# Performance work log

Hardware: AMD Instinct MI355X
Metric: run time of the kernel (lower is better)

Reference implementation:

```python
import jax, jax.numpy as jnp
import numpy as np

H = 2048      # hidden_size
I = 768       # moe_intermediate_size
E = 32        # num_experts
K = 8         # num_experts_per_tok (top_k)
T = 1024      # tokens (batch * seq)


def setup_inputs() -> dict:
    key = jax.random.key(0)
    k1, k2, k3, k4 = jax.random.split(key, 4)
    return {
        "hidden_states": jax.random.normal(k1, (T, H), jnp.float32),
        "gate_weight": jax.random.normal(k2, (E, H), jnp.float32) * 0.02,
        "w13_weight": jax.random.normal(k3, (E, 2 * I, H), jnp.float32) * 0.02,
        "w2_weight": jax.random.normal(k4, (E, H, I), jnp.float32) * 0.02,
    }


def reference(hidden_states, gate_weight, w13_weight, w2_weight):
    x = hidden_states  # [T, H]
    # --- router (Qwen3MoeSparseMoeBlock gating) ---
    logits = x @ gate_weight.T                      # [T, E]
    probs = jax.nn.softmax(logits, axis=-1)
    topk_w, topk_idx = jax.lax.top_k(probs, K)      # [T, K]
    topk_w = topk_w / jnp.sum(topk_w, axis=-1, keepdims=True)  # norm_topk_prob
    # dense combine matrix [T, E]: routing weight per (token, expert), 0 if not selected
    combine = jnp.zeros((x.shape[0], E), x.dtype).at[
        jnp.arange(x.shape[0])[:, None], topk_idx
    ].add(topk_w)
    # --- expert FFNs (fused gate+up = w13, SiLU-gated, then w2 down-proj) ---
    h = jnp.einsum('th,eoh->eto', x, w13_weight)    # [E, T, 2I]
    gate, up = h[:, :, :I], h[:, :, I:]
    act = jax.nn.silu(gate) * up                    # [E, T, I]
    y = jnp.einsum('eti,ehi->eth', act, w2_weight)  # [E, T, H]
    # --- weighted combine ---
    return jnp.einsum('eth,te->th', y, combine)     # [T, H]
```

## Files before the change

### kernel.cpp

```cpp
#include <hip/hip_runtime.h>
#include <hip/hip_bf16.h>
#include <math.h>

#define T_TOK 1024
#define H_DIM 2048
#define I_DIM 768
#define E_NUM 32
#define K_TOP 8
#define BK 32
#define GRID_P 1024

typedef __bf16 bf16x8 __attribute__((ext_vector_type(8)));
typedef float  f32x4  __attribute__((ext_vector_type(4)));

__device__ __forceinline__ bf16x8 cvt2_bf16(const f32x4 a, const f32x4 b) {
    bf16x8 r;
    r[0] = (__bf16)a[0]; r[1] = (__bf16)a[1]; r[2] = (__bf16)a[2]; r[3] = (__bf16)a[3];
    r[4] = (__bf16)b[0]; r[5] = (__bf16)b[1]; r[6] = (__bf16)b[2]; r[7] = (__bf16)b[3];
    return r;
}

__device__ __forceinline__ int frag_off(int r, int kgrp8) {
    return (r >> 4) * 512 + kgrp8 * 128 + (r & 15) * 8;
}

__global__ __launch_bounds__(256) void zero_kernel(float* __restrict__ p)
{
    const int i = (blockIdx.x * 256 + threadIdx.x) * 4;
    *(f32x4*)(p + i) = f32x4{0.f, 0.f, 0.f, 0.f};
}

__global__ __launch_bounds__(256) void cvtx_kernel(
    const float* __restrict__ x, __bf16* __restrict__ xb)
{
    const int i = (blockIdx.x * 256 + threadIdx.x) * 8;
    const f32x4 a = *(const f32x4*)(x + i);
    const f32x4 b = *(const f32x4*)(x + i + 4);
    *(bf16x8*)(xb + i) = cvt2_bf16(a, b);
}

__global__ __launch_bounds__(256) void router_kernel(
    const float* __restrict__ x, const float* __restrict__ gw,
    float* __restrict__ wdense, unsigned int* __restrict__ masks)
{
    const int t = blockIdx.x;
    const int tid = threadIdx.x;
    __shared__ float part[256];
    __shared__ float logits[E_NUM];
    const int e = tid & 31;
    const int chunk = tid >> 5;
    const float* xr = x + (size_t)t * H_DIM;
    const float* gr = gw + (size_t)e * H_DIM;
    const int base = chunk * (H_DIM / 8);
    float s = 0.f;
    for (int h = 0; h < H_DIM / 8; h += 4) {
        const f32x4 xv = *reinterpret_cast<const f32x4*>(xr + base + h);
        const f32x4 gv = *reinterpret_cast<const f32x4*>(gr + base + h);
        s += xv[0]*gv[0] + xv[1]*gv[1] + xv[2]*gv[2] + xv[3]*gv[3];
    }
    part[tid] = s;
    __syncthreads();
    if (tid < E_NUM) {
        float tot = 0.f;
        for (int c = 0; c < 8; ++c) tot += part[c * 32 + tid];
        logits[tid] = tot;
    }
    __syncthreads();
    if (tid == 0) {
        float l[E_NUM];
        for (int i = 0; i < E_NUM; ++i) {
            l[i] = logits[i];
            wdense[(size_t)t * E_NUM + i] = 0.f;
        }
        unsigned mask = 0;
        int   idx[K_TOP];
        float lv[K_TOP];
        for (int k = 0; k < K_TOP; ++k) {
            float best = -1e30f; int bi = 0;
            for (int i = 0; i < E_NUM; ++i)
                if (!((mask >> i) & 1u) && l[i] > best) { best = l[i]; bi = i; }
            mask |= (1u << bi); idx[k] = bi; lv[k] = best;
        }
        const float m = lv[0];
        float den = 0.f;
        for (int k = 0; k < K_TOP; ++k) den += expf(lv[k] - m);
        for (int k = 0; k < K_TOP; ++k)
            wdense[(size_t)t * E_NUM + idx[k]] = expf(lv[k] - m) / den;
        masks[t] = mask;
    }
}

__global__ __launch_bounds__(256) void count_kernel(
    const unsigned int* __restrict__ masks, int* __restrict__ cnt)
{
    const int e = blockIdx.x;
    const int tid = threadIdx.x;
    int c = 0;
    for (int t = tid; t < T_TOK; t += 256) c += (masks[t] >> e) & 1u;
    __shared__ int red[256];
    red[tid] = c; __syncthreads();
    for (int s = 128; s > 0; s >>= 1) {
        if (tid < s) red[tid] += red[tid + s];
        __syncthreads();
    }
    if (tid == 0) cnt[e] = red[0];
}

__global__ void scan_kernel(const int* __restrict__ cnt, int* __restrict__ off,
                            int* __restrict__ tbl)
{
    if (threadIdx.x == 0 && blockIdx.x == 0) {
        int r = 0, nt = 0;
        for (int e = 0; e < E_NUM; ++e) {
            off[e] = r;
            const int c = cnt[e];
            r += c;
            const int t = (c + 127) >> 7;
            for (int z = 0; z < t; ++z) tbl[1 + nt++] = (e << 8) | z;
        }
        tbl[0] = nt;
    }
}

__global__ __launch_bounds__(256) void fill_kernel(
    const unsigned int* __restrict__ masks, const float* __restrict__ wdense,
    const int* __restrict__ off, int* __restrict__ tok, float* __restrict__ wgt)
{
    const int e = blockIdx.x;
    const int tid = threadIdx.x;
    const int PER = T_TOK / 256;
    int sel[PER]; int c = 0;
    for (int i = 0; i < PER; ++i) {
        const int t = tid * PER + i;
        sel[i] = (masks[t] >> e) & 1u;
        c += sel[i];
    }
    __shared__ int s[256];
    s[tid] = c; __syncthreads();
    if (tid == 0) {
        int r = 0;
        for (int j = 0; j < 256; ++j) { int v = s[j]; s[j] = r; r += v; }
    }
    __syncthreads();
    int pos = off[e] + s[tid];
    for (int i = 0; i < PER; ++i) {
        if (sel[i]) {
            const int t = tid * PER + i;
            tok[pos] = t;
            wgt[pos] = wdense[(size_t)t * E_NUM + e];
            pos++;
        }
    }
}

#define G1_PHASE(P, Q)                                                         \
  {                                                                            \
    if (scur + 2 < NS) {                                                       \
      const int kk = (scur + 2) * BK;                                          \
      pa##P##_0 = *(const bf16x8*)(xp + kk);                                   \
      pa##P##_1 = *(const bf16x8*)(xp + kk + 8);                               \
      pb##P##_0 = *(const f32x4*)(wp + kk);                                    \
      pb##P##_1 = *(const f32x4*)(wp + kk + 4);                                \
      pb##P##_2 = *(const f32x4*)(wp + kk + 8);                                \
      pb##P##_3 = *(const f32x4*)(wp + kk + 12);                               \
    }                                                                          \
    bf16x8 af[4], bfr[4];                                                      \
    _Pragma("unroll")                                                          \
    for (int m = 0; m < 4; ++m)                                                \
      af[m] = *(const bf16x8*)&As[P][((wm >> 4) + m) * 512 + lane * 8];        \
    _Pragma("unroll")                                                          \
    for (int n = 0; n < 4; ++n)                                                \
      bfr[n] = *(const bf16x8*)&Bs[P][(wn * 4 + n) * 512 + lane * 8];          \
    _Pragma("unroll")                                                          \
    for (int m = 0; m < 4; ++m)                                                \
      _Pragma("unroll")                                                        \
      for (int n = 0; n < 4; ++n)                                              \
        acc[m][n] = __builtin_amdgcn_mfma_f32_16x16x32_bf16(af[m], bfr[n],     \
                                                            acc[m][n], 0,0,0); \
    if (scur + 1 < NS) {                                                       \
      *(bf16x8*)&As[Q][wo]       = pa##Q##_0;                                  \
      *(bf16x8*)&As[Q][wo + 128] = pa##Q##_1;                                  \
      *(bf16x8*)&Bs[Q][wo]       = cvt2_bf16(pb##Q##_0, pb##Q##_1);            \
      *(bf16x8*)&Bs[Q][wo + 128] = cvt2_bf16(pb##Q##_2, pb##Q##_3);            \
    }                                                                          \
    asm volatile("s_waitcnt lgkmcnt(0)" ::: "memory");                         \
    __builtin_amdgcn_s_barrier();                                              \
    ++scur;                                                                    \
  }

__global__ __launch_bounds__(256, 3) void gemm1_kernel(
    const __bf16* __restrict__ xb, const float* __restrict__ w13,
    const int* __restrict__ tok, const int* __restrict__ cnt,
    const int* __restrict__ off, const int* __restrict__ tbl,
    unsigned short* __restrict__ act)
{
    __shared__ __bf16 As[2][4096];
    __shared__ __bf16 Bs[2][4096];
    const int tid  = threadIdx.x;
    const int wid  = tid >> 6;
    const int lane = tid & 63;
    const int wm = (wid >> 1) * 64;
    const int wn = (wid & 1);
    const int lrow = lane & 15;
    const int sr = tid >> 1;
    const int kh = tid & 1;
    const int wo = frag_off(sr, kh * 2);
    const int NS = H_DIM / BK;

    const int W = tbl[0] * 12;
    for (int w = blockIdx.x; w < W; w += gridDim.x) {
        const int ti   = w / 12;
        const int nidx = w - ti * 12;
        const int ez = tbl[1 + ti];
        const int e  = ez >> 8;
        const int m0 = (ez & 255) * 128;
        const int c  = cnt[e];
        const int o  = off[e];
        const int n0 = nidx * 64;

        int rA = m0 + sr; rA = rA < c ? rA : c - 1;
        const __bf16* xp = xb + (size_t)tok[o + rA] * H_DIM + kh * 16;
        const int grp = sr >> 5;
        const int wrow = (grp & 1) * I_DIM + n0 + (grp >> 1) * 32 + (sr & 31);
        const float* wp = w13 + (size_t)e * (2 * I_DIM) * H_DIM
                              + (size_t)wrow * H_DIM + kh * 16;

        bf16x8 pa0_0, pa0_1, pa1_0, pa1_1;
        f32x4  pb0_0, pb0_1, pb0_2, pb0_3, pb1_0, pb1_1, pb1_2, pb1_3;
        f32x4  acc[4][4] = {};

        pa0_0 = *(const bf16x8*)(xp);
        pa0_1 = *(const bf16x8*)(xp + 8);
        pb0_0 = *(const f32x4*)(wp);
        pb0_1 = *(const f32x4*)(wp + 4);
        pb0_2 = *(const f32x4*)(wp + 8);
        pb0_3 = *(const f32x4*)(wp + 12);
        pa1_0 = *(const bf16x8*)(xp + BK);
        pa1_1 = *(const bf16x8*)(xp + BK + 8);
        pb1_0 = *(const f32x4*)(wp + BK);
        pb1_1 = *(const f32x4*)(wp + BK + 4);
        pb1_2 = *(const f32x4*)(wp + BK + 8);
        pb1_3 = *(const f32x4*)(wp + BK + 12);
        *(bf16x8*)&As[0][wo]       = pa0_0;
        *(bf16x8*)&As[0][wo + 128] = pa0_1;
        *(bf16x8*)&Bs[0][wo]       = cvt2_bf16(pb0_0, pb0_1);
        *(bf16x8*)&Bs[0][wo + 128] = cvt2_bf16(pb0_2, pb0_3);
        asm volatile("s_waitcnt lgkmcnt(0)" ::: "memory");
        __builtin_amdgcn_s_barrier();

        int scur = 0;
        for (int it = 0; it < NS; it += 2) {
            G1_PHASE(0, 1)
            G1_PHASE(1, 0)
        }

#pragma unroll
        for (int m = 0; m < 4; ++m)
#pragma unroll
            for (int n = 0; n < 2; ++n)
#pragma unroll
                for (int i = 0; i < 4; ++i) {
                    const int row = m0 + wm + m * 16 + (lane >> 4) * 4 + i;
                    if (row < c) {
                        const int icol = n0 + wn * 32 + n * 16 + lrow;
                        const float g = acc[m][n][i];
                        const float u = acc[m][n + 2][i];
                        const float a = (g / (1.f + expf(-g))) * u;
                        act[(size_t)(o + row) * I_DIM + icol] =
                            __builtin_bit_cast(unsigned short, (__bf16)a);
                    }
                }
    }
}

#define G2_PHASE(P, Q)                                                         \
  {                                                                            \
    if (scur + 2 < NS) {                                                       \
      const int kk = (scur + 2) * BK;                                          \
      qa##P##_0 = *(const bf16x8*)(ap + kk);                                   \
      qa##P##_1 = *(const bf16x8*)(ap + kk + 8);                               \
      qb##P##_0 = *(const f32x4*)(wp + kk);                                    \
      qb##P##_1 = *(const f32x4*)(wp + kk + 4);                                \
      qb##P##_2 = *(const f32x4*)(wp + kk + 8);                                \
      qb##P##_3 = *(const f32x4*)(wp + kk + 12);                               \
    }                                                                          \
    bf16x8 af[4], bfr[4];                                                      \
    _Pragma("unroll")                                                          \
    for (int m = 0; m < 4; ++m)                                                \
      af[m] = *(const bf16x8*)&As[P][((wm >> 4) + m) * 512 + lane * 8];        \
    _Pragma("unroll")                                                          \
    for (int n = 0; n < 4; ++n)                                                \
      bfr[n] = *(const bf16x8*)&Bs[P][(wn * 4 + n) * 512 + lane * 8];          \
    _Pragma("unroll")                                                          \
    for (int m = 0; m < 4; ++m)                                                \
      _Pragma("unroll")                                                        \
      for (int n = 0; n < 4; ++n)                                              \
        acc[m][n] = __builtin_amdgcn_mfma_f32_16x16x32_bf16(af[m], bfr[n],     \
                                                            acc[m][n], 0,0,0); \
    if (scur + 1 < NS) {                                                       \
      *(bf16x8*)&As[Q][wo]       = qa##Q##_0;                                  \
      *(bf16x8*)&As[Q][wo + 128] = qa##Q##_1;                                  \
      *(bf16x8*)&Bs[Q][wo]       = cvt2_bf16(qb##Q##_0, qb##Q##_1);            \
      *(bf16x8*)&Bs[Q][wo + 128] = cvt2_bf16(qb##Q##_2, qb##Q##_3);            \
    }                                                                          \
    asm volatile("s_waitcnt lgkmcnt(0)" ::: "memory");                         \
    __builtin_amdgcn_s_barrier();                                              \
    ++scur;                                                                    \
  }

__global__ __launch_bounds__(256, 3) void gemm2_kernel(
    const unsigned short* __restrict__ act, const float* __restrict__ w2,
    const int* __restrict__ tok, const float* __restrict__ wgt,
    const int* __restrict__ cnt, const int* __restrict__ off,
    const int* __restrict__ tbl, float* __restrict__ out)
{
    __shared__ __bf16 As[2][4096];
    __shared__ __bf16 Bs[2][4096];
    const int tid  = threadIdx.x;
    const int wid  = tid >> 6;
    const int lane = tid & 63;
    const int wm = (wid >> 1) * 64;
    const int wn = (wid & 1);
    const int lrow = lane & 15;
    const int sr = tid >> 1;
    const int kh = tid & 1;
    const int wo = frag_off(sr, kh * 2);
    const int NS = I_DIM / BK;

    const int W = tbl[0] * 16;
    for (int w = blockIdx.x; w < W; w += gridDim.x) {
        const int ti   = w >> 4;
        const int nidx = w & 15;
        const int ez = tbl[1 + ti];
        const int e  = ez >> 8;
        const int m0 = (ez & 255) * 128;
        const int c  = cnt[e];
        const int o  = off[e];
        const int n0 = nidx * 128;

        int rA = m0 + sr; rA = rA < c ? rA : c - 1;
        const __bf16* ap = (const __bf16*)act + (size_t)(o + rA) * I_DIM + kh * 16;
        const float* wp = w2 + (size_t)e * H_DIM * I_DIM
                             + (size_t)(n0 + sr) * I_DIM + kh * 16;

        bf16x8 qa0_0, qa0_1, qa1_0, qa1_1;
        f32x4  qb0_0, qb0_1, qb0_2, qb0_3, qb1_0, qb1_1, qb1_2, qb1_3;
        f32x4  acc[4][4] = {};

        qa0_0 = *(const bf16x8*)(ap);
        qa0_1 = *(const bf16x8*)(ap + 8);
        qb0_0 = *(const f32x4*)(wp);
        qb0_1 = *(const f32x4*)(wp + 4);
        qb0_2 = *(const f32x4*)(wp + 8);
        qb0_3 = *(const f32x4*)(wp + 12);
        qa1_0 = *(const bf16x8*)(ap + BK);
        qa1_1 = *(const bf16x8*)(ap + BK + 8);
        qb1_0 = *(const f32x4*)(wp + BK);
        qb1_1 = *(const f32x4*)(wp + BK + 4);
        qb1_2 = *(const f32x4*)(wp + BK + 8);
        qb1_3 = *(const f32x4*)(wp + BK + 12);
        *(bf16x8*)&As[0][wo]       = qa0_0;
        *(bf16x8*)&As[0][wo + 128] = qa0_1;
        *(bf16x8*)&Bs[0][wo]       = cvt2_bf16(qb0_0, qb0_1);
        *(bf16x8*)&Bs[0][wo + 128] = cvt2_bf16(qb0_2, qb0_3);
        asm volatile("s_waitcnt lgkmcnt(0)" ::: "memory");
        __builtin_amdgcn_s_barrier();

        int scur = 0;
        for (int it = 0; it < NS; it += 2) {
            G2_PHASE(0, 1)
            G2_PHASE(1, 0)
        }

#pragma unroll
        for (int m = 0; m < 4; ++m)
#pragma unroll
            for (int n = 0; n < 4; ++n)
#pragma unroll
                for (int i = 0; i < 4; ++i) {
                    const int row = m0 + wm + m * 16 + (lane >> 4) * 4 + i;
                    if (row < c) {
                        const int t = tok[o + row];
                        const float wv = wgt[o + row];
                        const int hcol = n0 + wn * 64 + n * 16 + lrow;
                        atomicAdd(&out[(size_t)t * H_DIM + hcol], wv * acc[m][n][i]);
                    }
                }
    }
}

extern "C" void kernel_launch(void* const* d_in, const int* in_sizes, int n_in,
                              void* d_out, int out_size, void* d_ws, size_t ws_size,
                              hipStream_t stream)
{
    const float* x   = (const float*)d_in[0];
    const float* gw  = (const float*)d_in[1];
    const float* w13 = (const float*)d_in[2];
    const float* w2  = (const float*)d_in[3];
    float* out = (float*)d_out;

    char* ws = (char*)d_ws;
    float*          wdense = (float*)(ws + 0x00000);
    unsigned int*   masks  = (unsigned int*)(ws + 0x20000);
    int*            cnt    = (int*)(ws + 0x21000);
    int*            off    = (int*)(ws + 0x21800);
    int*            tbl    = (int*)(ws + 0x22000);
    int*            tok    = (int*)(ws + 0x23000);
    float*          wgt    = (float*)(ws + 0x2B000);
    unsigned short* act    = (unsigned short*)(ws + 0x33000);
    __bf16*         xb     = (__bf16*)(ws + 0xC40000);

    zero_kernel<<<(T_TOK * H_DIM) / (256 * 4), 256, 0, stream>>>(out);

    cvtx_kernel<<<(T_TOK * H_DIM) / (256 * 8), 256, 0, stream>>>(x, xb);
    router_kernel<<<T_TOK, 256, 0, stream>>>(x, gw, wdense, masks);
    count_kernel<<<E_NUM, 256, 0, stream>>>(masks, cnt);
    scan_kernel<<<1, 64, 0, stream>>>(cnt, off, tbl);
    fill_kernel<<<E_NUM, 256, 0, stream>>>(masks, wdense, off, tok, wgt);
    gemm1_kernel<<<GRID_P, 256, 0, stream>>>(xb, w13, tok, cnt, off, tbl, act);
    gemm2_kernel<<<GRID_P, 256, 0, stream>>>(act, w2, tok, wgt, cnt, off, tbl, out);
}
```

Before: 384.5 us.

## Load A fragments directly from global into registers, swizzle B LDS layout

Both expert GEMMs now skip staging the activation (A) operand in shared memory. Each lane loads its MFMA A fragments straight from global memory into registers, double-buffered across k-steps. The B tile in LDS gets an XOR swizzle to reduce bank conflicts, gemm2's occupancy hint rises to 4, and gemm1's grid drops to 768 blocks. The aim is less LDS traffic and footprint, at the cost of redundant, less-coalesced global A loads across waves that share rows.

```diff
diff --git a/kernel.cpp b/kernel.cpp
--- a/kernel.cpp
+++ b/kernel.cpp
@@ -8,10 +8,11 @@
 #define E_NUM 32
 #define K_TOP 8
 #define BK 32
-#define GRID_P 1024
 
 typedef __bf16 bf16x8 __attribute__((ext_vector_type(8)));
 typedef float  f32x4  __attribute__((ext_vector_type(4)));
+
+#define MFMA16(a, b, c) __builtin_amdgcn_mfma_f32_16x16x32_bf16((a), (b), (c), 0, 0, 0)
 
 __device__ __forceinline__ bf16x8 cvt2_bf16(const f32x4 a, const f32x4 b) {
     bf16x8 r;
@@ -22,6 +23,9 @@
 
 __device__ __forceinline__ int frag_off(int r, int kgrp8) {
     return (r >> 4) * 512 + kgrp8 * 128 + (r & 15) * 8;
+}
+__device__ __forceinline__ int swz(int e) {
+    return e ^ (((e >> 8) & 3) << 3);
 }
 
 __global__ __launch_bounds__(256) void zero_kernel(float* __restrict__ p)
@@ -153,48 +157,67 @@
     }
 }
 
-#define G1_PHASE(P, Q)                                                         \
+#define GEMM_PHASE(P, Q)                                                       \
   {                                                                            \
+    bf16x8 bfr[4];                                                             \
+    _Pragma("unroll")                                                          \
+    for (int n = 0; n < 4; ++n)                                                \
+      bfr[n] = *(const bf16x8*)&Bs[P][swz((wn * 4 + n) * 512 + lane * 8)];     \
+    _Pragma("unroll")                                                          \
+    for (int n = 0; n < 4; ++n) {                                              \
+      acc[0][n] = MFMA16(a##P##0, bfr[n], acc[0][n]);                          \
+      acc[1][n] = MFMA16(a##P##1, bfr[n], acc[1][n]);                          \
+      acc[2][n] = MFMA16(a##P##2, bfr[n], acc[2][n]);                          \
+      acc[3][n] = MFMA16(a##P##3, bfr[n], acc[3][n]);                          \
+    }                                                                          \
     if (scur + 2 < NS) {                                                       \
       const int kk = (scur + 2) * BK;                                          \
-      pa##P##_0 = *(const bf16x8*)(xp + kk);                                   \
-      pa##P##_1 = *(const bf16x8*)(xp + kk + 8);                               \
-      pb##P##_0 = *(const f32x4*)(wp + kk);                                    \
-      pb##P##_1 = *(const f32x4*)(wp + kk + 4);                                \
-      pb##P##_2 = *(const f32x4*)(wp + kk + 8);                                \
-      pb##P##_3 = *(const f32x4*)(wp + kk + 12);                               \
+      a##P##0 = *(const bf16x8*)(arp0 + kk);                                   \
+      a##P##1 = *(const bf16x8*)(arp1 + kk);                                   \
+      a##P##2 = *(const bf16x8*)(arp2 + kk);                                   \
+      a##P##3 = *(const bf16x8*)(arp3 + kk);                                   \
+      pb##P##0 = *(const f32x4*)(wp + kk);                                     \
+      pb##P##1 = *(const f32x4*)(wp + kk + 4);                                 \
+      pb##P##2 = *(const f32x4*)(wp + kk + 8);                                 \
+      pb##P##3 = *(const f32x4*)(wp + kk + 12);                                \
     }                                                                          \
-    bf16x8 af[4], bfr[4];                                                      \
-    _Pragma("unroll")                                                          \
-    for (int m = 0; m < 4; ++m)                                                \
-      af[m] = *(const bf16x8*)&As[P][((wm >> 4) + m) * 512 + lane * 8];        \
-    _Pragma("unroll")                                                          \
-    for (int n = 0; n < 4; ++n)                                                \
-      bfr[n] = *(const bf16x8*)&Bs[P][(wn * 4 + n) * 512 + lane * 8];          \
-    _Pragma("unroll")                                                          \
-    for (int m = 0; m < 4; ++m)                                                \
-      _Pragma("unroll")                                                        \
-      for (int n = 0; n < 4; ++n)                                              \
-        acc[m][n] = __builtin_amdgcn_mfma_f32_16x16x32_bf16(af[m], bfr[n],     \
-                                                            acc[m][n], 0,0,0); \
     if (scur + 1 < NS) {                                                       \
-      *(bf16x8*)&As[Q][wo]       = pa##Q##_0;                                  \
-      *(bf16x8*)&As[Q][wo + 128] = pa##Q##_1;                                  \
-      *(bf16x8*)&Bs[Q][wo]       = cvt2_bf16(pb##Q##_0, pb##Q##_1);            \
-      *(bf16x8*)&Bs[Q][wo + 128] = cvt2_bf16(pb##Q##_2, pb##Q##_3);            \
+      *(bf16x8*)&Bs[Q][swz(wo)]       = cvt2_bf16(pb##Q##0, pb##Q##1);         \
+      *(bf16x8*)&Bs[Q][swz(wo + 128)] = cvt2_bf16(pb##Q##2, pb##Q##3);         \
     }                                                                          \
     asm volatile("s_waitcnt lgkmcnt(0)" ::: "memory");                         \
     __builtin_amdgcn_s_barrier();                                              \
     ++scur;                                                                    \
   }
 
+#define GEMM_PROLOGUE()                                                        \
+    a00 = *(const bf16x8*)(arp0);                                              \
+    a01 = *(const bf16x8*)(arp1);                                              \
+    a02 = *(const bf16x8*)(arp2);                                              \
+    a03 = *(const bf16x8*)(arp3);                                              \
+    pb00 = *(const f32x4*)(wp);                                                \
+    pb01 = *(const f32x4*)(wp + 4);                                            \
+    pb02 = *(const f32x4*)(wp + 8);                                            \
+    pb03 = *(const f32x4*)(wp + 12);                                           \
+    a10 = *(const bf16x8*)(arp0 + BK);                                         \
+    a11 = *(const bf16x8*)(arp1 + BK);                                         \
+    a12 = *(const bf16x8*)(arp2 + BK);                                         \
+    a13 = *(const bf16x8*)(arp3 + BK);                                         \
+    pb10 = *(const f32x4*)(wp + BK);                                           \
+    pb11 = *(const f32x4*)(wp + BK + 4);                                       \
+    pb12 = *(const f32x4*)(wp + BK + 8);                                       \
+    pb13 = *(const f32x4*)(wp + BK + 12);                                      \
+    *(bf16x8*)&Bs[0][swz(wo)]       = cvt2_bf16(pb00, pb01);                   \
+    *(bf16x8*)&Bs[0][swz(wo + 128)] = cvt2_bf16(pb02, pb03);                   \
+    asm volatile("s_waitcnt lgkmcnt(0)" ::: "memory");                         \
+    __builtin_amdgcn_s_barrier();
+
 __global__ __launch_bounds__(256, 3) void gemm1_kernel(
     const __bf16* __restrict__ xb, const float* __restrict__ w13,
     const int* __restrict__ tok, const int* __restrict__ cnt,
     const int* __restrict__ off, const int* __restrict__ tbl,
     unsigned short* __restrict__ act)
 {
-    __shared__ __bf16 As[2][4096];
     __shared__ __bf16 Bs[2][4096];
     const int tid  = threadIdx.x;
     const int wid  = tid >> 6;
@@ -218,40 +241,33 @@
         const int o  = off[e];
         const int n0 = nidx * 64;
 
-        int rA = m0 + sr; rA = rA < c ? rA : c - 1;
-        const __bf16* xp = xb + (size_t)tok[o + rA] * H_DIM + kh * 16;
+        const __bf16 *arp0, *arp1, *arp2, *arp3;
+        {
+            int r0 = m0 + wm + 0  + lrow; r0 = r0 < c ? r0 : c - 1;
+            int r1 = m0 + wm + 16 + lrow; r1 = r1 < c ? r1 : c - 1;
+            int r2 = m0 + wm + 32 + lrow; r2 = r2 < c ? r2 : c - 1;
+            int r3 = m0 + wm + 48 + lrow; r3 = r3 < c ? r3 : c - 1;
+            const int kq = (lane >> 4) * 8;
+            arp0 = xb + (size_t)tok[o + r0] * H_DIM + kq;
+            arp1 = xb + (size_t)tok[o + r1] * H_DIM + kq;
+            arp2 = xb + (size_t)tok[o + r2] * H_DIM + kq;
+            arp3 = xb + (size_t)tok[o + r3] * H_DIM + kq;
+        }
         const int grp = sr >> 5;
         const int wrow = (grp & 1) * I_DIM + n0 + (grp >> 1) * 32 + (sr & 31);
         const float* wp = w13 + (size_t)e * (2 * I_DIM) * H_DIM
                               + (size_t)wrow * H_DIM + kh * 16;
 
-        bf16x8 pa0_0, pa0_1, pa1_0, pa1_1;
-        f32x4  pb0_0, pb0_1, pb0_2, pb0_3, pb1_0, pb1_1, pb1_2, pb1_3;
+        bf16x8 a00, a01, a02, a03, a10, a11, a12, a13;
+        f32x4  pb00, pb01, pb02, pb03, pb10, pb11, pb12, pb13;
         f32x4  acc[4][4] = {};
 
-        pa0_0 = *(const bf16x8*)(xp);
-        pa0_1 = *(const bf16x8*)(xp + 8);
-        pb0_0 = *(const f32x4*)(wp);
-        pb0_1 = *(const f32x4*)(wp + 4);
-        pb0_2 = *(const f32x4*)(wp + 8);
-        pb0_3 = *(const f32x4*)(wp + 12);
-        pa1_0 = *(const bf16x8*)(xp + BK);
-        pa1_1 = *(const bf16x8*)(xp + BK + 8);
-        pb1_0 = *(const f32x4*)(wp + BK);
-        pb1_1 = *(const f32x4*)(wp + BK + 4);
-        pb1_2 = *(const f32x4*)(wp + BK + 8);
-        pb1_3 = *(const f32x4*)(wp + BK + 12);
-        *(bf16x8*)&As[0][wo]       = pa0_0;
-        *(bf16x8*)&As[0][wo + 128] = pa0_1;
-        *(bf16x8*)&Bs[0][wo]       = cvt2_bf16(pb0_0, pb0_1);
-        *(bf16x8*)&Bs[0][wo + 128] = cvt2_bf16(pb0_2, pb0_3);
-        asm volatile("s_waitcnt lgkmcnt(0)" ::: "memory");
-        __builtin_amdgcn_s_barrier();
+        GEMM_PROLOGUE()
 
         int scur = 0;
         for (int it = 0; it < NS; it += 2) {
-            G1_PHASE(0, 1)
-            G1_PHASE(1, 0)
+            GEMM_PHASE(0, 1)
+            GEMM_PHASE(1, 0)
         }
 
 #pragma unroll
@@ -273,48 +289,12 @@
     }
 }
 
-#define G2_PHASE(P, Q)                                                         \
-  {                                                                            \
-    if (scur + 2 < NS) {                                                       \
-      const int kk = (scur + 2) * BK;                                          \
-      qa##P##_0 = *(const bf16x8*)(ap + kk);                                   \
-      qa##P##_1 = *(const bf16x8*)(ap + kk + 8);                               \
-      qb##P##_0 = *(const f32x4*)(wp + kk);                                    \
-      qb##P##_1 = *(const f32x4*)(wp + kk + 4);                                \
-      qb##P##_2 = *(const f32x4*)(wp + kk + 8);                                \
-      qb##P##_3 = *(const f32x4*)(wp + kk + 12);                               \
-    }                                                                          \
-    bf16x8 af[4], bfr[4];                                                      \
-    _Pragma("unroll")                                                          \
-    for (int m = 0; m < 4; ++m)                                                \
-      af[m] = *(const bf16x8*)&As[P][((wm >> 4) + m) * 512 + lane * 8];        \
-    _Pragma("unroll")                                                          \
-    for (int n = 0; n < 4; ++n)                                                \
-      bfr[n] = *(const bf16x8*)&Bs[P][(wn * 4 + n) * 512 + lane * 8];          \
-    _Pragma("unroll")                                                          \
-    for (int m = 0; m < 4; ++m)                                                \
-      _Pragma("unroll")                                                        \
-      for (int n = 0; n < 4; ++n)                                              \
-        acc[m][n] = __builtin_amdgcn_mfma_f32_16x16x32_bf16(af[m], bfr[n],     \
-                                                            acc[m][n], 0,0,0); \
-    if (scur + 1 < NS) {                                                       \
-      *(bf16x8*)&As[Q][wo]       = qa##Q##_0;                                  \
-      *(bf16x8*)&As[Q][wo + 128] = qa##Q##_1;                                  \
-      *(bf16x8*)&Bs[Q][wo]       = cvt2_bf16(qb##Q##_0, qb##Q##_1);            \
-      *(bf16x8*)&Bs[Q][wo + 128] = cvt2_bf16(qb##Q##_2, qb##Q##_3);            \
-    }                                                                          \
-    asm volatile("s_waitcnt lgkmcnt(0)" ::: "memory");                         \
-    __builtin_amdgcn_s_barrier();                                              \
-    ++scur;                                                                    \
-  }
-
-__global__ __launch_bounds__(256, 3) void gemm2_kernel(
+__global__ __launch_bounds__(256, 4) void gemm2_kernel(
     const unsigned short* __restrict__ act, const float* __restrict__ w2,
     const int* __restrict__ tok, const float* __restrict__ wgt,
     const int* __restrict__ cnt, const int* __restrict__ off,
     const int* __restrict__ tbl, float* __restrict__ out)
 {
-    __shared__ __bf16 As[2][4096];
     __shared__ __bf16 Bs[2][4096];
     const int tid  = threadIdx.x;
     const int wid  = tid >> 6;
@@ -338,38 +318,31 @@
         const int o  = off[e];
         const int n0 = nidx * 128;
 
-        int rA = m0 + sr; rA = rA < c ? rA : c - 1;
-        const __bf16* ap = (const __bf16*)act + (size_t)(o + rA) * I_DIM + kh * 16;
+        const __bf16 *arp0, *arp1, *arp2, *arp3;
+        {
+            int r0 = m0 + wm + 0  + lrow; r0 = r0 < c ? r0 : c - 1;
+            int r1 = m0 + wm + 16 + lrow; r1 = r1 < c ? r1 : c - 1;
+            int r2 = m0 + wm + 32 + lrow; r2 = r2 < c ? r2 : c - 1;
+            int r3 = m0 + wm + 48 + lrow; r3 = r3 < c ? r3 : c - 1;
+            const int kq = (lane >> 4) * 8;
+            arp0 = (const __bf16*)act + (size_t)(o + r0) * I_DIM + kq;
+            arp1 = (const __bf16*)act + (size_t)(o + r1) * I_DIM + kq;
+            arp2 = (const __bf16*)act + (size_t)(o + r2) * I_DIM + kq;
+            arp3 = (const __bf16*)act + (size_t)(o + r3) * I_DIM + kq;
+        }
         const float* wp = w2 + (size_t)e * H_DIM * I_DIM
                              + (size_t)(n0 + sr) * I_DIM + kh * 16;
 
-        bf16x8 qa0_0, qa0_1, qa1_0, qa1_1;
-        f32x4  qb0_0, qb0_1, qb0_2, qb0_3, qb1_0, qb1_1, qb1_2, qb1_3;
+        bf16x8 a00, a01, a02, a03, a10, a11, a12, a13;
+        f32x4  pb00, pb01, pb02, pb03, pb10, pb11, pb12, pb13;
         f32x4  acc[4][4] = {};
 
-        qa0_0 = *(const bf16x8*)(ap);
-        qa0_1 = *(const bf16x8*)(ap + 8);
-        qb0_0 = *(const f32x4*)(wp);
-        qb0_1 = *(const f32x4*)(wp + 4);
-        qb0_2 = *(const f32x4*)(wp + 8);
-        qb0_3 = *(const f32x4*)(wp + 12);
-        qa1_0 = *(const bf16x8*)(ap + BK);
-        qa1_1 = *(const bf16x8*)(ap + BK + 8);
-        qb1_0 = *(const f32x4*)(wp + BK);
-        qb1_1 = *(const f32x4*)(wp + BK + 4);
-        qb1_2 = *(const f32x4*)(wp + BK + 8);
-        qb1_3 = *(const f32x4*)(wp + BK + 12);
-        *(bf16x8*)&As[0][wo]       = qa0_0;
-        *(bf16x8*)&As[0][wo + 128] = qa0_1;
-        *(bf16x8*)&Bs[0][wo]       = cvt2_bf16(qb0_0, qb0_1);
-        *(bf16x8*)&Bs[0][wo + 128] = cvt2_bf16(qb0_2, qb0_3);
-        asm volatile("s_waitcnt lgkmcnt(0)" ::: "memory");
-        __builtin_amdgcn_s_barrier();
+        GEMM_PROLOGUE()
 
         int scur = 0;
         for (int it = 0; it < NS; it += 2) {
-            G2_PHASE(0, 1)
-            G2_PHASE(1, 0)
+            GEMM_PHASE(0, 1)
+            GEMM_PHASE(1, 0)
         }
 
 #pragma unroll
@@ -411,12 +384,11 @@
     __bf16*         xb     = (__bf16*)(ws + 0xC40000);
 
     zero_kernel<<<(T_TOK * H_DIM) / (256 * 4), 256, 0, stream>>>(out);
-
     cvtx_kernel<<<(T_TOK * H_DIM) / (256 * 8), 256, 0, stream>>>(x, xb);
     router_kernel<<<T_TOK, 256, 0, stream>>>(x, gw, wdense, masks);
     count_kernel<<<E_NUM, 256, 0, stream>>>(masks, cnt);
     scan_kernel<<<1, 64, 0, stream>>>(cnt, off, tbl);
     fill_kernel<<<E_NUM, 256, 0, stream>>>(masks, wdense, off, tok, wgt);
-    gemm1_kernel<<<GRID_P, 256, 0, stream>>>(xb, w13, tok, cnt, off, tbl, act);
-    gemm2_kernel<<<GRID_P, 256, 0, stream>>>(act, w2, tok, wgt, cnt, off, tbl, out);
-}
+    gemm1_kernel<<<768, 256, 0, stream>>>(xb, w13, tok, cnt, off, tbl, act);
+    gemm2_kernel<<<1024, 256, 0, stream>>>(act, w2, tok, wgt, cnt, off, tbl, out);
+}
```

Result: slower. 642.9 us (+67.2%).
